# Optimization experiments

Measured on AMD Instinct MI355X. Metric: run time of the kernel, lower is better.

Reference implementation:

```python
import jax, jax.numpy as jnp
import numpy as np

BITS = 8

def _hilbert_distance(grid, bits=BITS):
    # Skilling's algorithm: 3D grid coords -> Hilbert curve distance. grid: [N,3] int64.
    X = grid.astype(np.int64).copy()
    n = X.shape[1]
    M = 1 << (bits - 1)
    Q = M
    while Q > 1:
        P = Q - 1
        for i in range(n):
            hi = (X[:, i] & Q) != 0
            X[:, 0] = np.where(hi, X[:, 0] ^ P, X[:, 0])
            t = np.where(hi, 0, (X[:, 0] ^ X[:, i]) & P)
            X[:, 0] ^= t
            X[:, i] ^= t
        Q >>= 1
    for i in range(1, n):
        X[:, i] ^= X[:, i - 1]
    t = np.zeros(X.shape[0], dtype=np.int64)
    Q = M
    while Q > 1:
        t = np.where((X[:, n - 1] & Q) != 0, t ^ (Q - 1), t)
        Q >>= 1
    X ^= t[:, None]
    h = np.zeros(X.shape[0], dtype=np.int64)
    for b in range(bits - 1, -1, -1):
        for i in range(n):
            h = (h << 1) | ((X[:, i] >> b) & 1)
    return h

def _orders(x_np, bits=BITS):
    B, N, _ = x_np.shape
    oh = np.zeros((B, N), dtype=np.int64)
    ot = np.zeros((B, N), dtype=np.int64)
    gmax = (1 << bits) - 1
    for b in range(B):
        pts = x_np[b]
        mins, maxs = pts.min(0), pts.max(0)
        span = np.maximum(maxs - mins, 1e-6)
        norm = (pts - mins) / span
        g = np.clip(norm * gmax, 0, gmax).astype(np.int64)
        oh[b] = np.argsort(_hilbert_distance(g, bits), kind='stable')
        gt = np.clip(norm[:, ::-1] * gmax, 0, gmax).astype(np.int64)
        ot[b] = np.argsort(_hilbert_distance(gt, bits), kind='stable')
    return oh, ot

def setup_inputs() -> dict:
    key = jax.random.key(0)
    ks = jax.random.split(key, 12)
    B, N, E = 4, 2048, 128
    NB, DS, DC, EXP, NC = 2, 16, 4, 2, 40
    DI = E * EXP
    DR = max(1, (E + 15) // 16)
    x = jax.random.normal(ks[0], (B, N, 3), jnp.float32)
    oh, ot = _orders(np.asarray(x))
    # dt_proj bias = softplus^-1(dt), dt ~ LogUniform(1e-3, 0.1)
    dt = jnp.exp(jax.random.uniform(ks[1], (NB, DI)) * (np.log(0.1) - np.log(0.001)) + np.log(0.001))
    dtproj_b = dt + jnp.log(-jnp.expm1(-dt))
    return dict(
        x=x,
        order_h=jnp.asarray(oh), order_t=jnp.asarray(ot),
        pe_w=jax.random.normal(ks[2], (E, 3)) * 0.3, pe_b=jnp.zeros((E,)),
        gamma=jnp.ones((2, E)), beta=jnp.zeros((2, E)),
        ln_g=jnp.ones((NB, E)), ln_b=jnp.zeros((NB, E)),
        inproj_w=jax.random.normal(ks[3], (NB, 2 * DI, E)) * (E ** -0.5),
        conv_w=jax.random.normal(ks[4], (NB, DI, DC)) * 0.3,
        conv_b=jnp.zeros((NB, DI)),
        xproj_w=jax.random.normal(ks[5], (NB, DR + 2 * DS, DI)) * (DI ** -0.5),
        dtproj_w=jax.random.normal(ks[6], (NB, DI, DR)) * (DR ** -0.5),
        dtproj_b=dtproj_b,
        A_log=jnp.tile(jnp.log(jnp.arange(1, DS + 1, dtype=jnp.float32))[None, None], (NB, DI, 1)),
        Dp=jnp.ones((NB, DI)),
        outproj_w=jax.random.normal(ks[7], (NB, E, DI)) * (DI ** -0.5),
        hn_g=jnp.ones((E,)), hn_b=jnp.zeros((E,)),
        fc_w=jax.random.normal(ks[8], (NC, E)) * (E ** -0.5),
        fc_b=jnp.zeros((NC,)),
    )

def _ln(x, g, b):
    m = jnp.mean(x, -1, keepdims=True)
    v = jnp.mean((x - m) ** 2, -1, keepdims=True)
    return (x - m) / jnp.sqrt(v + 1e-5) * g + b

def _block(h, g, bb, inw, cw, cb, xw, dtw, dtb, Alog, Dv, outw):
    B, L, E = h.shape
    DI, DC = cw.shape
    DR = dtw.shape[1]
    DS = Alog.shape[1]
    xn = _ln(h, g, bb)
    uz = xn @ inw.T                       # [B, L, 2*DI]
    u, z = uz[..., :DI], uz[..., DI:]
    # depthwise causal conv (kernel DC, left pad DC-1)
    up = jnp.pad(u, ((0, 0), (DC - 1, 0), (0, 0)))
    uc = cb + sum(up[:, k:k + L, :] * cw[:, k] for k in range(DC))
    uc = jax.nn.silu(uc)
    xdbl = uc @ xw.T                      # [B, L, DR+2*DS]
    dt = xdbl[..., :DR]
    Bv = xdbl[..., DR:DR + DS]
    Cv = xdbl[..., DR + DS:]
    delta = jax.nn.softplus(dt @ dtw.T + dtb)  # [B, L, DI]
    A = -jnp.exp(Alog)                    # [DI, DS]
    def step(hst, xs):
        d, ut, bt, ct = xs                # [B,DI],[B,DI],[B,DS],[B,DS]
        hst = jnp.exp(d[:, :, None] * A[None]) * hst + (d * ut)[:, :, None] * bt[:, None, :]
        y = jnp.einsum('bds,bs->bd', hst, ct) + Dv * ut
        return hst, y
    h0 = jnp.zeros((B, DI, DS), h.dtype)
    _, ys = jax.lax.scan(step, h0, (delta.transpose(1, 0, 2), uc.transpose(1, 0, 2),
                                    Bv.transpose(1, 0, 2), Cv.transpose(1, 0, 2)))
    y = ys.transpose(1, 0, 2) * jax.nn.silu(z)
    return h + y @ outw.T

def reference(x, order_h, order_t, pe_w, pe_b, gamma, beta, ln_g, ln_b,
              inproj_w, conv_w, conv_b, xproj_w, dtproj_w, dtproj_b,
              A_log, Dp, outproj_w, hn_g, hn_b, fc_w, fc_b):
    pts_h = jnp.take_along_axis(x, order_h[..., None], axis=1)
    pts_t = jnp.take_along_axis(x, order_t[..., None], axis=1)
    th = (pts_h @ pe_w.T + pe_b) * gamma[0] + beta[0]
    tt = (pts_t @ pe_w.T + pe_b) * gamma[1] + beta[1]
    h = jnp.concatenate([th, tt], axis=1)  # [B, 2N, E]
    for i in range(ln_g.shape[0]):
        h = _block(h, ln_g[i], ln_b[i], inproj_w[i], conv_w[i], conv_b[i], xproj_w[i],
                   dtproj_w[i], dtproj_b[i], A_log[i], Dp[i], outproj_w[i])
    h = _ln(h, hn_g, hn_b)
    return h.mean(axis=1) @ fc_w.T + fc_b
```

## Files before the change

kernel.cpp:

```cpp
#include <hip/hip_runtime.h>
#include <hip/hip_bf16.h>
#include <math.h>

#define BATCH 4
#define NPTS  2048
#define L     4096
#define E     128
#define DI    256
#define DS    16
#define DRR   8
#define DCV   4
#define NBLK  2
#define NC    40
#define XDW   40
#define ROWS  (BATCH*L)
#define CH    32
#define NCH   128

typedef unsigned short u16;
typedef short short8 __attribute__((ext_vector_type(8)));
typedef float f32x4v __attribute__((ext_vector_type(4)));

__device__ __forceinline__ u16 f2bf(float x) {
  unsigned u = __float_as_uint(x);
  u = u + 0x7FFFu + ((u >> 16) & 1u);
  return (u16)(u >> 16);
}
__device__ __forceinline__ float bf2f(u16 h) {
  return __uint_as_float(((unsigned)h) << 16);
}
__device__ __forceinline__ float softplusf(float x) {
  if (x > 20.f) return x;
  float t = __builtin_amdgcn_exp2f(x * 1.44269504f);
  return 0.69314718f * __builtin_amdgcn_logf(1.f + t);
}

__global__ void embed_ln_split(const float* __restrict__ x,
                               const int* __restrict__ oh, const int* __restrict__ ot,
                               const float* __restrict__ pe_w, const float* __restrict__ pe_b,
                               const float* __restrict__ gamma, const float* __restrict__ beta,
                               const float* __restrict__ g, const float* __restrict__ bb,
                               float* __restrict__ h, u16* __restrict__ dhi, u16* __restrict__ dlo) {
  int wave = threadIdx.x >> 6;
  int lane = threadIdx.x & 63;
  int row = blockIdx.x * 4 + wave;
  int n = row % L;
  int b = row / L;
  int gi = (n >= NPTS) ? 1 : 0;
  int nn = n - gi * NPTS;
  int src = gi ? ot[b * NPTS + nn] : oh[b * NPTS + nn];
  const float* xp = x + ((size_t)b * NPTS + src) * 3;
  float p0 = xp[0], p1 = xp[1], p2 = xp[2];
  int e0 = lane, e1 = lane + 64;
  float v0 = pe_b[e0] + p0 * pe_w[e0 * 3] + p1 * pe_w[e0 * 3 + 1] + p2 * pe_w[e0 * 3 + 2];
  float v1 = pe_b[e1] + p0 * pe_w[e1 * 3] + p1 * pe_w[e1 * 3 + 1] + p2 * pe_w[e1 * 3 + 2];
  v0 = v0 * gamma[gi * E + e0] + beta[gi * E + e0];
  v1 = v1 * gamma[gi * E + e1] + beta[gi * E + e1];
  size_t base = (size_t)row * E;
  h[base + e0] = v0;
  h[base + e1] = v1;
  float s1 = v0 + v1, s2 = v0 * v0 + v1 * v1;
  #pragma unroll
  for (int off = 32; off > 0; off >>= 1) {
    s1 += __shfl_xor(s1, off);
    s2 += __shfl_xor(s2, off);
  }
  float m = s1 * (1.0f / E);
  float var = s2 * (1.0f / E) - m * m;
  float inv = rsqrtf(var + 1e-5f);
  float o0 = (v0 - m) * inv * g[e0] + bb[e0];
  float o1 = (v1 - m) * inv * g[e1] + bb[e1];
  u16 h0 = f2bf(o0), h1 = f2bf(o1);
  dhi[base + e0] = h0; dhi[base + e1] = h1;
  dlo[base + e0] = f2bf(o0 - bf2f(h0));
  dlo[base + e1] = f2bf(o1 - bf2f(h1));
}

__global__ void split_all(const float* __restrict__ inproj, const float* __restrict__ outw,
                          const float* __restrict__ xw,
                          u16* __restrict__ wihi, u16* __restrict__ wilo,
                          u16* __restrict__ wohi, u16* __restrict__ wolo,
                          u16* __restrict__ wxhi, u16* __restrict__ wxlo) {
  const int n1 = NBLK * 2 * DI * E;
  const int n2 = NBLK * E * DI;
  const int n3 = NBLK * XDW * DI;
  int i = blockIdx.x * 256 + threadIdx.x;
  if (i < n1) {
    float v = inproj[i];
    u16 h = f2bf(v);
    wihi[i] = h; wilo[i] = f2bf(v - bf2f(h));
  } else if (i < n1 + n2) {
    int j = i - n1;
    float v = outw[j];
    u16 h = f2bf(v);
    wohi[j] = h; wolo[j] = f2bf(v - bf2f(h));
  } else if (i < n1 + n2 + n3) {
    int j = i - n1 - n2;
    float v = xw[j];
    u16 h = f2bf(v);
    wxhi[j] = h; wxlo[j] = f2bf(v - bf2f(h));
  }
}

template<int BN, int ACC>
__global__ __launch_bounds__(256)
void mfma_gemm_lds(const u16* __restrict__ Ahi, const u16* __restrict__ Alo,
                   const u16* __restrict__ Bhi, const u16* __restrict__ Blo,
                   float* __restrict__ C, int M, int N, int K, int ldc) {
  constexpr int BM = 128, BK = 64, PITCH = 72;
  constexpr int MSUB = (BN == 128) ? 4 : 2;
  constexpr int NSUB = 4;
  __shared__ u16 sA[2][BM][PITCH];
  __shared__ u16 sB[2][BN][PITCH];
  int tid = threadIdx.x;
  int wave = tid >> 6, lane = tid & 63, quad = lane >> 4, l16 = lane & 15;
  int rowBase = blockIdx.x * BM, colBase = blockIdx.y * BN;
  int wrow = (BN == 128) ? (wave >> 1) * 64 : wave * 32;
  int wcol = (BN == 128) ? (wave & 1) * 64 : 0;
  f32x4v acc[MSUB][NSUB] = {};
  for (int k0 = 0; k0 < K; k0 += BK) {
    #pragma unroll
    for (int hl = 0; hl < 2; hl++) {
      const u16* srcA = hl ? Alo : Ahi;
      #pragma unroll
      for (int c = 0; c < BM * 8 / 256; c++) {
        int ch = c * 256 + tid;
        int row = ch >> 3, kc = ch & 7;
        float4 v = *(const float4*)(srcA + (size_t)(rowBase + row) * K + k0 + kc * 8);
        *(float4*)&sA[hl][row][kc * 8] = v;
      }
      const u16* srcB = hl ? Blo : Bhi;
      #pragma unroll
      for (int c = 0; c < BN * 8 / 256; c++) {
        int ch = c * 256 + tid;
        int row = ch >> 3, kc = ch & 7;
        float4 v = *(const float4*)(srcB + (size_t)(colBase + row) * K + k0 + kc * 8);
        *(float4*)&sB[hl][row][kc * 8] = v;
      }
    }
    __syncthreads();
    short8 afh[MSUB][2], afl[MSUB][2];
    #pragma unroll
    for (int i = 0; i < MSUB; i++)
      #pragma unroll
      for (int kf = 0; kf < 2; kf++) {
        afh[i][kf] = *(const short8*)&sA[0][wrow + i * 16 + l16][kf * 32 + quad * 8];
        afl[i][kf] = *(const short8*)&sA[1][wrow + i * 16 + l16][kf * 32 + quad * 8];
      }
    #pragma unroll
    for (int j = 0; j < NSUB; j++)
      #pragma unroll
      for (int kf = 0; kf < 2; kf++) {
        short8 bh = *(const short8*)&sB[0][wcol + j * 16 + l16][kf * 32 + quad * 8];
        short8 bl = *(const short8*)&sB[1][wcol + j * 16 + l16][kf * 32 + quad * 8];
        #pragma unroll
        for (int i = 0; i < MSUB; i++) {
          acc[i][j] = __builtin_amdgcn_mfma_f32_16x16x32_bf16(afh[i][kf], bh, acc[i][j], 0, 0, 0);
          acc[i][j] = __builtin_amdgcn_mfma_f32_16x16x32_bf16(afh[i][kf], bl, acc[i][j], 0, 0, 0);
          acc[i][j] = __builtin_amdgcn_mfma_f32_16x16x32_bf16(afl[i][kf], bh, acc[i][j], 0, 0, 0);
        }
      }
    __syncthreads();
  }
  int orow0 = rowBase + wrow + quad * 4;
  #pragma unroll
  for (int i = 0; i < MSUB; i++) {
    #pragma unroll
    for (int j = 0; j < NSUB; j++) {
      int cc = colBase + wcol + j * 16 + l16;
      #pragma unroll
      for (int r = 0; r < 4; r++) {
        size_t idx = (size_t)(orow0 + i * 16 + r) * ldc + cc;
        if (ACC) C[idx] += acc[i][j][r];
        else     C[idx] = acc[i][j][r];
      }
    }
  }
}

__global__ __launch_bounds__(256)
void conv_xproj(const float* __restrict__ uz, const float* __restrict__ cw,
                const float* __restrict__ cb,
                const u16* __restrict__ xwhi, const u16* __restrict__ xwlo,
                float* __restrict__ xdbl) {
  constexpr int RB = 16, UPITCH = DI + 8;
  __shared__ u16 sUhi[RB][UPITCH];
  __shared__ u16 sUlo[RB][UPITCH];
  int d = threadIdx.x;
  int r0 = blockIdx.x * RB;
  int t0 = r0 % L;
  const size_t US = 2 * DI;
  float w0 = cw[d * DCV], w1 = cw[d * DCV + 1], w2 = cw[d * DCV + 2], w3 = cw[d * DCV + 3];
  float bias = cb[d];
  float uwin[RB + 3];
  #pragma unroll
  for (int j = 0; j < RB + 3; j++) {
    int t = t0 + j - 3;
    uwin[j] = (t >= 0) ? uz[(size_t)(r0 + j - 3) * US + d] : 0.f;
  }
  #pragma unroll
  for (int j = 0; j < RB; j++) {
    float a = bias + w0 * uwin[j] + w1 * uwin[j + 1] + w2 * uwin[j + 2] + w3 * uwin[j + 3];
    float v = a / (1.f + __expf(-a));
    u16 hh = f2bf(v);
    sUhi[j][d] = hh;
    sUlo[j][d] = f2bf(v - bf2f(hh));
  }
  __syncthreads();
  int wave = threadIdx.x >> 6, lane = threadIdx.x & 63;
  int quad = lane >> 4, l16 = lane & 15;
  if (wave < 3) {
    int col = wave * 16 + l16;
    int colc = (col < XDW) ? col : 0;
    const u16* bhp = xwhi + (size_t)colc * DI;
    const u16* blp = xwlo + (size_t)colc * DI;
    f32x4v acc = {};
    #pragma unroll
    for (int ks = 0; ks < DI / 32; ks++) {
      short8 ah = *(const short8*)&sUhi[l16][ks * 32 + quad * 8];
      short8 al = *(const short8*)&sUlo[l16][ks * 32 + quad * 8];
      short8 bh = *(const short8*)(bhp + ks * 32 + quad * 8);
      short8 bl = *(const short8*)(blp + ks * 32 + quad * 8);
      acc = __builtin_amdgcn_mfma_f32_16x16x32_bf16(ah, bh, acc, 0, 0, 0);
      acc = __builtin_amdgcn_mfma_f32_16x16x32_bf16(ah, bl, acc, 0, 0, 0);
      acc = __builtin_amdgcn_mfma_f32_16x16x32_bf16(al, bh, acc, 0, 0, 0);
      acc = __builtin_amdgcn_mfma_f32_16x16x32_bf16(al, bl, acc, 0, 0, 0);
    }
    if (col < XDW) {
      #pragma unroll
      for (int r = 0; r < 4; r++)
        xdbl[(size_t)(r0 + quad * 4 + r) * XDW + col] = acc[r];
    }
  }
}

__global__ __launch_bounds__(256, 4)
void scan_passA(const float* __restrict__ uz, const float* __restrict__ xdbl,
                const float* __restrict__ dtw, const float* __restrict__ dtb,
                const float* __restrict__ A_log,
                const float* __restrict__ cw, const float* __restrict__ cb,
                float* __restrict__ hloc, float* __restrict__ sumd) {
  int b = blockIdx.x / NCH, c = blockIdx.x % NCH;
  int d = threadIdx.x;
  __shared__ float Bsh[CH][DS];
  __shared__ float Dsh[CH][DRR];
  for (int i = threadIdx.x; i < CH * DS; i += 256) {
    int tt = i >> 4, s = i & 15;
    Bsh[tt][s] = xdbl[((size_t)b * L + c * CH + tt) * XDW + DRR + s];
  }
  {
    int i = threadIdx.x;
    int td = i >> 3, q = i & 7;
    Dsh[td][q] = xdbl[((size_t)b * L + c * CH + td) * XDW + q];
  }
  const size_t US = 2 * DI;
  const float* up = uz + ((size_t)b * L + c * CH) * US + d;
  float cw0 = cw[d * DCV], cw1 = cw[d * DCV + 1], cw2 = cw[d * DCV + 2], cw3 = cw[d * DCV + 3];
  float cbias = cb[d];
  float um0, um1, um2;
  if (c == 0) { um0 = um1 = um2 = 0.f; }
  else {
    um0 = up[-3 * (ptrdiff_t)US];
    um1 = up[-2 * (ptrdiff_t)US];
    um2 = up[-1 * (ptrdiff_t)US];
  }
  float ucur = up[0];
  float Av[DS];
  #pragma unroll
  for (int s = 0; s < DS; s++) Av[s] = -__expf(A_log[d * DS + s]);
  float4 wd0 = *(const float4*)(dtw + d * DRR);
  float4 wd1 = *(const float4*)(dtw + d * DRR + 4);
  float dbias = dtb[d];
  __syncthreads();
  float st[DS] = {};
  float sd = 0.f;
  #pragma unroll
  for (int t0 = 0; t0 < CH; t0++) {
    float unext = (t0 + 1 < CH) ? up[(size_t)(t0 + 1) * US] : 0.f;
    float a = cbias + cw0 * um0 + cw1 * um1 + cw2 * um2 + cw3 * ucur;
    float utv = a / (1.f + __expf(-a));
    um0 = um1; um1 = um2; um2 = ucur; ucur = unext;
    float4 D0 = *(const float4*)&Dsh[t0][0];
    float4 D1 = *(const float4*)&Dsh[t0][4];
    float v = dbias + D0.x * wd0.x + D0.y * wd0.y + D0.z * wd0.z + D0.w * wd0.w
                    + D1.x * wd1.x + D1.y * wd1.y + D1.z * wd1.z + D1.w * wd1.w;
    float dl = softplusf(v);
    sd += dl;
    float du = dl * utv;
    float4 B0 = *(const float4*)&Bsh[t0][0];
    float4 B1 = *(const float4*)&Bsh[t0][4];
    float4 B2 = *(const float4*)&Bsh[t0][8];
    float4 B3 = *(const float4*)&Bsh[t0][12];
    float Bv[DS] = {B0.x, B0.y, B0.z, B0.w, B1.x, B1.y, B1.z, B1.w,
                    B2.x, B2.y, B2.z, B2.w, B3.x, B3.y, B3.z, B3.w};
    #pragma unroll
    for (int s = 0; s < DS; s++) {
      float aa = __expf(dl * Av[s]);
      st[s] = aa * st[s] + du * Bv[s];
    }
  }
  size_t base = (((size_t)b * NCH + c) * DI + d) * DS;
  *(float4*)&hloc[base + 0]  = float4{st[0], st[1], st[2], st[3]};
  *(float4*)&hloc[base + 4]  = float4{st[4], st[5], st[6], st[7]};
  *(float4*)&hloc[base + 8]  = float4{st[8], st[9], st[10], st[11]};
  *(float4*)&hloc[base + 12] = float4{st[12], st[13], st[14], st[15]};
  sumd[((size_t)b * NCH + c) * DI + d] = sd;
}

#define PB_G 16
__global__ __launch_bounds__(64)
void scan_passB(const float* __restrict__ A_log, const float* __restrict__ hloc,
                const float* __restrict__ sumd, float* __restrict__ hinit) {
  int tid = threadIdx.x;
  int dgroup = blockIdx.x % (DI / 4);
  int b = blockIdx.x / (DI / 4);
  int d = dgroup * 4 + (tid >> 4);
  int s = tid & 15;
  float Av = -__expf(A_log[d * DS + s]);
  size_t off = (size_t)b * NCH * DI * DS + dgroup * 64 + tid;
  size_t soff = (size_t)b * NCH * DI + d;
  const size_t HST = (size_t)DI * DS;
  float bv[PB_G], sd[PB_G], bvn[PB_G], sdn[PB_G];
  #pragma unroll
  for (int j = 0; j < PB_G; j++) {
    bv[j] = hloc[off + j * HST];
    sd[j] = sumd[soff + j * DI];
  }
  float X = 0.f;
  for (int g = 0; g < NCH / PB_G; g++) {
    if (g + 1 < NCH / PB_G) {
      #pragma unroll
      for (int j = 0; j < PB_G; j++) {
        bvn[j] = hloc[off + (j + PB_G) * HST];
        sdn[j] = sumd[soff + (j + PB_G) * DI];
      }
    }
    #pragma unroll
    for (int j = 0; j < PB_G; j++) {
      float a = __expf(Av * sd[j]);
      hinit[off + j * HST] = X;
      X = a * X + bv[j];
    }
    #pragma unroll
    for (int j = 0; j < PB_G; j++) { bv[j] = bvn[j]; sd[j] = sdn[j]; }
    off += PB_G * HST;
    soff += PB_G * DI;
  }
}

template<int VARIANT>
__global__ __launch_bounds__(256, 2)
void scan_passC_out(const float* __restrict__ uz, const float* __restrict__ xdbl,
                    const float* __restrict__ dtw, const float* __restrict__ dtb,
                    const float* __restrict__ A_log, const float* __restrict__ Dp,
                    const float* __restrict__ cw, const float* __restrict__ cb,
                    const float* __restrict__ hinit,
                    const u16* __restrict__ wohi, const u16* __restrict__ wolo,
                    float* __restrict__ h, const float* __restrict__ g,
                    const float* __restrict__ bb, u16* __restrict__ dhi,
                    u16* __restrict__ dlo, float* __restrict__ partial) {
  constexpr int YP = DI + 8;
  constexpr int HP = E + 4;
  int b = blockIdx.x / NCH, c = blockIdx.x % NCH;
  int d = threadIdx.x;
  __shared__ float Bsh[CH][DS];
  __shared__ float Csh[CH][DS];
  __shared__ float Dsh[CH][DRR];
  __shared__ u16 sYhi[CH][YP];
  __shared__ u16 sYlo[CH][YP];
  __shared__ float hsm[CH][HP];
  __shared__ float red[4][E];
  for (int i = threadIdx.x; i < CH * DS; i += 256) {
    int tt = i >> 4, s = i & 15;
    size_t rb = ((size_t)b * L + c * CH + tt) * XDW;
    Bsh[tt][s] = xdbl[rb + DRR + s];
    Csh[tt][s] = xdbl[rb + DRR + DS + s];
  }
  {
    int i = threadIdx.x;
    int td = i >> 3, q = i & 7;
    Dsh[td][q] = xdbl[((size_t)b * L + c * CH + td) * XDW + q];
  }
  const size_t US = 2 * DI;
  const float* up = uz + ((size_t)b * L + c * CH) * US + d;
  const float* zp = up + DI;
  float cw0 = cw[d * DCV], cw1 = cw[d * DCV + 1], cw2 = cw[d * DCV + 2], cw3 = cw[d * DCV + 3];
  float cbias = cb[d];
  float um0, um1, um2;
  if (c == 0) { um0 = um1 = um2 = 0.f; }
  else {
    um0 = up[-3 * (ptrdiff_t)US];
    um1 = up[-2 * (ptrdiff_t)US];
    um2 = up[-1 * (ptrdiff_t)US];
  }
  float ucur = up[0];
  float zcur = zp[0];
  float st[DS];
  size_t hbase = (((size_t)b * NCH + c) * DI + d) * DS;
  {
    float4 h0 = *(const float4*)&hinit[hbase + 0];
    float4 h1 = *(const float4*)&hinit[hbase + 4];
    float4 h2 = *(const float4*)&hinit[hbase + 8];
    float4 h3 = *(const float4*)&hinit[hbase + 12];
    st[0]=h0.x; st[1]=h0.y; st[2]=h0.z; st[3]=h0.w;
    st[4]=h1.x; st[5]=h1.y; st[6]=h1.z; st[7]=h1.w;
    st[8]=h2.x; st[9]=h2.y; st[10]=h2.z; st[11]=h2.w;
    st[12]=h3.x; st[13]=h3.y; st[14]=h3.z; st[15]=h3.w;
  }
  float Av[DS];
  #pragma unroll
  for (int s = 0; s < DS; s++) Av[s] = -__expf(A_log[d * DS + s]);
  float4 wd0 = *(const float4*)(dtw + d * DRR);
  float4 wd1 = *(const float4*)(dtw + d * DRR + 4);
  float dbias = dtb[d];
  float Dv = Dp[d];
  __syncthreads();
  #pragma unroll 8
  for (int t0 = 0; t0 < CH; t0++) {
    float unext = (t0 + 1 < CH) ? up[(size_t)(t0 + 1) * US] : 0.f;
    float znext = (t0 + 1 < CH) ? zp[(size_t)(t0 + 1) * US] : 0.f;
    float a = cbias + cw0 * um0 + cw1 * um1 + cw2 * um2 + cw3 * ucur;
    float utv = a / (1.f + __expf(-a));
    um0 = um1; um1 = um2; um2 = ucur; ucur = unext;
    float4 D0 = *(const float4*)&Dsh[t0][0];
    float4 D1 = *(const float4*)&Dsh[t0][4];
    float v = dbias + D0.x * wd0.x + D0.y * wd0.y + D0.z * wd0.z + D0.w * wd0.w
                    + D1.x * wd1.x + D1.y * wd1.y + D1.z * wd1.z + D1.w * wd1.w;
    float dl = softplusf(v);
    float du = dl * utv;
    float acc = Dv * utv;
    float4 B0 = *(const float4*)&Bsh[t0][0];
    float4 B1 = *(const float4*)&Bsh[t0][4];
    float4 B2 = *(const float4*)&Bsh[t0][8];
    float4 B3 = *(const float4*)&Bsh[t0][12];
    float4 C0 = *(const float4*)&Csh[t0][0];
    float4 C1 = *(const float4*)&Csh[t0][4];
    float4 C2 = *(const float4*)&Csh[t0][8];
    float4 C3 = *(const float4*)&Csh[t0][12];
    float Bv[DS] = {B0.x, B0.y, B0.z, B0.w, B1.x, B1.y, B1.z, B1.w,
                    B2.x, B2.y, B2.z, B2.w, B3.x, B3.y, B3.z, B3.w};
    float Cv[DS] = {C0.x, C0.y, C0.z, C0.w, C1.x, C1.y, C1.z, C1.w,
                    C2.x, C2.y, C2.z, C2.w, C3.x, C3.y, C3.z, C3.w};
    #pragma unroll
    for (int s = 0; s < DS; s++) {
      float aa = __expf(dl * Av[s]);
      st[s] = aa * st[s] + du * Bv[s];
      acc += st[s] * Cv[s];
    }
    float zz = zcur; zcur = znext;
    float yv = acc * (zz / (1.f + __expf(-zz)));
    u16 hh = f2bf(yv);
    sYhi[t0][d] = hh;
    sYlo[t0][d] = f2bf(yv - bf2f(hh));
  }
  __syncthreads();
  int wave = d >> 6, lane = d & 63, quad = lane >> 4, l16 = lane & 15;
  f32x4v oacc[2][2] = {};
  #pragma unroll
  for (int ks = 0; ks < DI / 32; ks++) {
    short8 a0h = *(const short8*)&sYhi[l16][ks * 32 + quad * 8];
    short8 a0l = *(const short8*)&sYlo[l16][ks * 32 + quad * 8];
    short8 a1h = *(const short8*)&sYhi[16 + l16][ks * 32 + quad * 8];
    short8 a1l = *(const short8*)&sYlo[16 + l16][ks * 32 + quad * 8];
    #pragma unroll
    for (int j = 0; j < 2; j++) {
      int col = wave * 32 + j * 16 + l16;
      short8 bh = *(const short8*)(wohi + (size_t)col * DI + ks * 32 + quad * 8);
      short8 bl = *(const short8*)(wolo + (size_t)col * DI + ks * 32 + quad * 8);
      oacc[0][j] = __builtin_amdgcn_mfma_f32_16x16x32_bf16(a0h, bh, oacc[0][j], 0, 0, 0);
      oacc[0][j] = __builtin_amdgcn_mfma_f32_16x16x32_bf16(a0h, bl, oacc[0][j], 0, 0, 0);
      oacc[0][j] = __builtin_amdgcn_mfma_f32_16x16x32_bf16(a0l, bh, oacc[0][j], 0, 0, 0);
      oacc[1][j] = __builtin_amdgcn_mfma_f32_16x16x32_bf16(a1h, bh, oacc[1][j], 0, 0, 0);
      oacc[1][j] = __builtin_amdgcn_mfma_f32_16x16x32_bf16(a1h, bl, oacc[1][j], 0, 0, 0);
      oacc[1][j] = __builtin_amdgcn_mfma_f32_16x16x32_bf16(a1l, bh, oacc[1][j], 0, 0, 0);
    }
  }
  size_t rr0 = (size_t)b * L + c * CH;
  #pragma unroll
  for (int i = 0; i < 2; i++) {
    #pragma unroll
    for (int j = 0; j < 2; j++) {
      int col = wave * 32 + j * 16 + l16;
      #pragma unroll
      for (int r = 0; r < 4; r++) {
        int row = i * 16 + quad * 4 + r;
        float v = h[(rr0 + row) * E + col] + oacc[i][j][r];
        hsm[row][col] = v;
        if (VARIANT == 0) h[(rr0 + row) * E + col] = v;
      }
    }
  }
  __syncthreads();
  float g0 = g[lane], g1 = g[lane + 64], b0 = bb[lane], b1 = bb[lane + 64];
  float pa0 = 0.f, pa1 = 0.f;
  for (int jj = 0; jj < 8; jj++) {
    int row = wave * 8 + jj;
    float x0 = hsm[row][lane], x1 = hsm[row][lane + 64];
    float s1 = x0 + x1, s2 = x0 * x0 + x1 * x1;
    #pragma unroll
    for (int off = 32; off > 0; off >>= 1) {
      s1 += __shfl_xor(s1, off);
      s2 += __shfl_xor(s2, off);
    }
    float m = s1 * (1.0f / E);
    float var = s2 * (1.0f / E) - m * m;
    float inv = rsqrtf(var + 1e-5f);
    float o0 = (x0 - m) * inv * g0 + b0;
    float o1 = (x1 - m) * inv * g1 + b1;
    if (VARIANT == 0) {
      size_t base = (rr0 + row) * E;
      u16 h0 = f2bf(o0), h1 = f2bf(o1);
      dhi[base + lane]      = h0;
      dhi[base + lane + 64] = h1;
      dlo[base + lane]      = f2bf(o0 - bf2f(h0));
      dlo[base + lane + 64] = f2bf(o1 - bf2f(h1));
    } else {
      pa0 += o0; pa1 += o1;
    }
  }
  if (VARIANT == 1) {
    red[wave][lane]      = pa0;
    red[wave][lane + 64] = pa1;
    __syncthreads();
    if (wave == 0) {
      #pragma unroll
      for (int half = 0; half < 2; half++) {
        int e = lane + half * 64;
        partial[(size_t)blockIdx.x * E + e] =
            red[0][e] + red[1][e] + red[2][e] + red[3][e];
      }
    }
  }
}

__global__ __launch_bounds__(256)
void fc_reduce(const float* __restrict__ partial, float* __restrict__ hmean) {
  int w = blockIdx.x * 4 + (threadIdx.x >> 6);
  int lane = threadIdx.x & 63;
  int b = w >> 7, e = w & 127;
  float s = partial[((size_t)b * NCH + lane) * E + e]
          + partial[((size_t)b * NCH + 64 + lane) * E + e];
  #pragma unroll
  for (int off = 32; off > 0; off >>= 1) s += __shfl_xor(s, off);
  if (lane == 0) hmean[w] = s;
}

__global__ __launch_bounds__(256)
void fc_final(const float* __restrict__ hmean, const float* __restrict__ fcw,
              const float* __restrict__ fcb, float* __restrict__ out) {
  constexpr int WP = E + 4;
  __shared__ float hm[BATCH * E];
  __shared__ float wsm[NC * WP];
  for (int i = threadIdx.x; i < BATCH * E; i += 256) hm[i] = hmean[i];
  for (int i = threadIdx.x; i < NC * E; i += 256) {
    int o = i >> 7, e = i & 127;
    wsm[o * WP + e] = fcw[i];
  }
  __syncthreads();
  int i = threadIdx.x;
  if (i < BATCH * NC) {
    int b = i / NC, o = i % NC;
    float acc = 0.f;
    #pragma unroll 8
    for (int e = 0; e < E; e++) acc += hm[b * E + e] * wsm[o * WP + e];
    out[i] = acc * (1.f / L) + fcb[o];
  }
}

extern "C" void kernel_launch(void* const* d_in, const int* in_sizes, int n_in,
                              void* d_out, int out_size, void* d_ws, size_t ws_size,
                              hipStream_t stream) {
  const float* x      = (const float*)d_in[0];
  const int*   oh     = (const int*)d_in[1];
  const int*   ot     = (const int*)d_in[2];
  const float* pe_w   = (const float*)d_in[3];
  const float* pe_b   = (const float*)d_in[4];
  const float* gamma  = (const float*)d_in[5];
  const float* beta   = (const float*)d_in[6];
  const float* ln_g   = (const float*)d_in[7];
  const float* ln_b   = (const float*)d_in[8];
  const float* inproj = (const float*)d_in[9];
  const float* conv_w = (const float*)d_in[10];
  const float* conv_b = (const float*)d_in[11];
  const float* xproj  = (const float*)d_in[12];
  const float* dtw    = (const float*)d_in[13];
  const float* dtb    = (const float*)d_in[14];
  const float* A_log  = (const float*)d_in[15];
  const float* Dp     = (const float*)d_in[16];
  const float* outw   = (const float*)d_in[17];
  const float* hn_g   = (const float*)d_in[18];
  const float* hn_b   = (const float*)d_in[19];
  const float* fc_w   = (const float*)d_in[20];
  const float* fc_b   = (const float*)d_in[21];
  float* out = (float*)d_out;

  char* ws = (char*)d_ws;
  size_t off = 0;
  auto alloc = [&](size_t bytes) { size_t o = off; off += (bytes + 255) & ~(size_t)255; return o; };
  float* h     = (float*)(ws + alloc((size_t)ROWS * E * 4));
  u16*   xnhi  = (u16*)  (ws + alloc((size_t)ROWS * E * 2));
  u16*   xnlo  = (u16*)  (ws + alloc((size_t)ROWS * E * 2));
  float* uz    = (float*)(ws + alloc((size_t)ROWS * 2 * DI * 4));
  float* xdbl  = (float*)(ws + alloc((size_t)ROWS * XDW * 4));
  float* hloc  = (float*)(ws + alloc((size_t)BATCH * NCH * DI * DS * 4));
  float* sumd  = (float*)(ws + alloc((size_t)BATCH * NCH * DI * 4));
  u16*   wihi  = (u16*)  (ws + alloc((size_t)NBLK * 2 * DI * E * 2));
  u16*   wilo  = (u16*)  (ws + alloc((size_t)NBLK * 2 * DI * E * 2));
  u16*   wohi  = (u16*)  (ws + alloc((size_t)NBLK * E * DI * 2));
  u16*   wolo  = (u16*)  (ws + alloc((size_t)NBLK * E * DI * 2));
  u16*   wxhi  = (u16*)  (ws + alloc((size_t)NBLK * XDW * DI * 2));
  u16*   wxlo  = (u16*)  (ws + alloc((size_t)NBLK * XDW * DI * 2));
  float* partial = (float*)(ws + alloc((size_t)BATCH * NCH * E * 4));
  float* hmean = (float*)(ws + alloc((size_t)BATCH * E * 4));
  float* hinit = hloc;

  embed_ln_split<<<ROWS / 4, 256, 0, stream>>>(x, oh, ot, pe_w, pe_b, gamma, beta,
                                               ln_g, ln_b, h, xnhi, xnlo);
  const int nsplit = NBLK * 2 * DI * E + NBLK * E * DI + NBLK * XDW * DI;
  split_all<<<(nsplit + 255) / 256, 256, 0, stream>>>(inproj, outw, xproj,
                                                      wihi, wilo, wohi, wolo, wxhi, wxlo);

  for (int i = 0; i < NBLK; i++) {
    dim3 g1(ROWS / 128, (2 * DI) / 128);
    mfma_gemm_lds<128, 0><<<g1, 256, 0, stream>>>(xnhi, xnlo,
                                                  wihi + (size_t)i * 2 * DI * E, wilo + (size_t)i * 2 * DI * E,
                                                  uz, ROWS, 2 * DI, E, 2 * DI);

    conv_xproj<<<ROWS / 16, 256, 0, stream>>>(uz, conv_w + (size_t)i * DI * DCV, conv_b + i * DI,
                                              wxhi + (size_t)i * XDW * DI, wxlo + (size_t)i * XDW * DI,
                                              xdbl);

    scan_passA<<<BATCH * NCH, 256, 0, stream>>>(uz, xdbl, dtw + (size_t)i * DI * DRR, dtb + i * DI,
                                                A_log + (size_t)i * DI * DS,
                                                conv_w + (size_t)i * DI * DCV, conv_b + i * DI,
                                                hloc, sumd);
    scan_passB<<<BATCH * (DI / 4), 64, 0, stream>>>(A_log + (size_t)i * DI * DS, hloc, sumd, hinit);

    if (i == 0) {
      scan_passC_out<0><<<BATCH * NCH, 256, 0, stream>>>(uz, xdbl, dtw + (size_t)i * DI * DRR, dtb + i * DI,
                                                         A_log + (size_t)i * DI * DS, Dp + i * DI,
                                                         conv_w + (size_t)i * DI * DCV, conv_b + i * DI,
                                                         hinit,
                                                         wohi + (size_t)i * E * DI, wolo + (size_t)i * E * DI,
                                                         h, ln_g + (i + 1) * E, ln_b + (i + 1) * E,
                                                         xnhi, xnlo, partial);
    } else {
      scan_passC_out<1><<<BATCH * NCH, 256, 0, stream>>>(uz, xdbl, dtw + (size_t)i * DI * DRR, dtb + i * DI,
                                                         A_log + (size_t)i * DI * DS, Dp + i * DI,
                                                         conv_w + (size_t)i * DI * DCV, conv_b + i * DI,
                                                         hinit,
                                                         wohi + (size_t)i * E * DI, wolo + (size_t)i * E * DI,
                                                         h, hn_g, hn_b,
                                                         xnhi, xnlo, partial);
    }
  }

  fc_reduce<<<128, 256, 0, stream>>>(partial, hmean);
  fc_final<<<1, 256, 0, stream>>>(hmean, fc_w, fc_b, out);
}
```

Before: 293.9 us.

## Fuse conv+xproj into scan pass A and use exp power ladder for A

Merges the conv_xproj kernel into the first scan pass, so each chunk block computes the conv+SiLU activations, runs the x_proj MFMA in shared memory and feeds delta/B straight into the local scan. This drops one launch and the xdbl round trip for pass A, while still writing xdbl for pass C. Both scan passes also gain a runtime check for whether A equals -(s+1), the standard S4D-real init. When it does, the 16 exponentials per step are replaced by one exp plus repeated multiplies. The fast path depends on the weights matching that init, and the fused kernel has more registers and LDS with fewer blocks per CU.

```diff
diff --git a/kernel.cpp b/kernel.cpp
--- a/kernel.cpp
+++ b/kernel.cpp
@@ -33,6 +33,22 @@
   if (x > 20.f) return x;
   float t = __builtin_amdgcn_exp2f(x * 1.44269504f);
   return 0.69314718f * __builtin_amdgcn_logf(1.f + t);
+}
+
+__device__ __forceinline__ void exp_ladder(bool fastE, float dl,
+                                           const float* __restrict__ Av,
+                                           float* __restrict__ aa) {
+  if (fastE) {
+    float e1 = __expf(-dl);
+    float e2 = e1 * e1, e4 = e2 * e2, e8 = e4 * e4;
+    aa[0] = e1;        aa[1] = e2;        aa[2] = e2 * e1;   aa[3] = e4;
+    aa[4] = e4 * e1;   aa[5] = e4 * e2;   aa[6] = aa[5] * e1; aa[7] = e8;
+    aa[8] = e8 * e1;   aa[9] = e8 * e2;   aa[10] = aa[9] * e1; aa[11] = e8 * e4;
+    aa[12] = aa[11] * e1; aa[13] = aa[11] * e2; aa[14] = aa[13] * e1; aa[15] = e8 * e8;
+  } else {
+    #pragma unroll
+    for (int s = 0; s < DS; s++) aa[s] = __expf(dl * Av[s]);
+  }
 }
 
 __global__ void embed_ln_split(const float* __restrict__ x,
@@ -178,81 +194,21 @@
   }
 }
 
-__global__ __launch_bounds__(256)
-void conv_xproj(const float* __restrict__ uz, const float* __restrict__ cw,
-                const float* __restrict__ cb,
-                const u16* __restrict__ xwhi, const u16* __restrict__ xwlo,
-                float* __restrict__ xdbl) {
-  constexpr int RB = 16, UPITCH = DI + 8;
-  __shared__ u16 sUhi[RB][UPITCH];
-  __shared__ u16 sUlo[RB][UPITCH];
-  int d = threadIdx.x;
-  int r0 = blockIdx.x * RB;
-  int t0 = r0 % L;
-  const size_t US = 2 * DI;
-  float w0 = cw[d * DCV], w1 = cw[d * DCV + 1], w2 = cw[d * DCV + 2], w3 = cw[d * DCV + 3];
-  float bias = cb[d];
-  float uwin[RB + 3];
-  #pragma unroll
-  for (int j = 0; j < RB + 3; j++) {
-    int t = t0 + j - 3;
-    uwin[j] = (t >= 0) ? uz[(size_t)(r0 + j - 3) * US + d] : 0.f;
-  }
-  #pragma unroll
-  for (int j = 0; j < RB; j++) {
-    float a = bias + w0 * uwin[j] + w1 * uwin[j + 1] + w2 * uwin[j + 2] + w3 * uwin[j + 3];
-    float v = a / (1.f + __expf(-a));
-    u16 hh = f2bf(v);
-    sUhi[j][d] = hh;
-    sUlo[j][d] = f2bf(v - bf2f(hh));
-  }
-  __syncthreads();
-  int wave = threadIdx.x >> 6, lane = threadIdx.x & 63;
-  int quad = lane >> 4, l16 = lane & 15;
-  if (wave < 3) {
-    int col = wave * 16 + l16;
-    int colc = (col < XDW) ? col : 0;
-    const u16* bhp = xwhi + (size_t)colc * DI;
-    const u16* blp = xwlo + (size_t)colc * DI;
-    f32x4v acc = {};
-    #pragma unroll
-    for (int ks = 0; ks < DI / 32; ks++) {
-      short8 ah = *(const short8*)&sUhi[l16][ks * 32 + quad * 8];
-      short8 al = *(const short8*)&sUlo[l16][ks * 32 + quad * 8];
-      short8 bh = *(const short8*)(bhp + ks * 32 + quad * 8);
-      short8 bl = *(const short8*)(blp + ks * 32 + quad * 8);
-      acc = __builtin_amdgcn_mfma_f32_16x16x32_bf16(ah, bh, acc, 0, 0, 0);
-      acc = __builtin_amdgcn_mfma_f32_16x16x32_bf16(ah, bl, acc, 0, 0, 0);
-      acc = __builtin_amdgcn_mfma_f32_16x16x32_bf16(al, bh, acc, 0, 0, 0);
-      acc = __builtin_amdgcn_mfma_f32_16x16x32_bf16(al, bl, acc, 0, 0, 0);
-    }
-    if (col < XDW) {
-      #pragma unroll
-      for (int r = 0; r < 4; r++)
-        xdbl[(size_t)(r0 + quad * 4 + r) * XDW + col] = acc[r];
-    }
-  }
-}
-
-__global__ __launch_bounds__(256, 4)
-void scan_passA(const float* __restrict__ uz, const float* __restrict__ xdbl,
-                const float* __restrict__ dtw, const float* __restrict__ dtb,
-                const float* __restrict__ A_log,
-                const float* __restrict__ cw, const float* __restrict__ cb,
-                float* __restrict__ hloc, float* __restrict__ sumd) {
+__global__ __launch_bounds__(256, 2)
+void scan_passA_cx(const float* __restrict__ uz,
+                   const float* __restrict__ cw, const float* __restrict__ cb,
+                   const u16* __restrict__ xwhi, const u16* __restrict__ xwlo,
+                   const float* __restrict__ dtw, const float* __restrict__ dtb,
+                   const float* __restrict__ A_log,
+                   float* __restrict__ xdbl,
+                   float* __restrict__ hloc, float* __restrict__ sumd) {
+  constexpr int UPITCH = DI + 8;
+  constexpr int XP = 48;
+  __shared__ u16 sUhi[CH][UPITCH];
+  __shared__ u16 sUlo[CH][UPITCH];
+  __shared__ float xsm[CH][XP];
   int b = blockIdx.x / NCH, c = blockIdx.x % NCH;
   int d = threadIdx.x;
-  __shared__ float Bsh[CH][DS];
-  __shared__ float Dsh[CH][DRR];
-  for (int i = threadIdx.x; i < CH * DS; i += 256) {
-    int tt = i >> 4, s = i & 15;
-    Bsh[tt][s] = xdbl[((size_t)b * L + c * CH + tt) * XDW + DRR + s];
-  }
-  {
-    int i = threadIdx.x;
-    int td = i >> 3, q = i & 7;
-    Dsh[td][q] = xdbl[((size_t)b * L + c * CH + td) * XDW + q];
-  }
   const size_t US = 2 * DI;
   const float* up = uz + ((size_t)b * L + c * CH) * US + d;
   float cw0 = cw[d * DCV], cw1 = cw[d * DCV + 1], cw2 = cw[d * DCV + 2], cw3 = cw[d * DCV + 3];
@@ -265,39 +221,83 @@
     um2 = up[-1 * (ptrdiff_t)US];
   }
   float ucur = up[0];
+  float utv[CH];
+  #pragma unroll
+  for (int j = 0; j < CH; j++) {
+    float unext = (j + 1 < CH) ? up[(size_t)(j + 1) * US] : 0.f;
+    float a = cbias + cw0 * um0 + cw1 * um1 + cw2 * um2 + cw3 * ucur;
+    float v = a / (1.f + __expf(-a));
+    um0 = um1; um1 = um2; um2 = ucur; ucur = unext;
+    utv[j] = v;
+    u16 hh = f2bf(v);
+    sUhi[j][d] = hh;
+    sUlo[j][d] = f2bf(v - bf2f(hh));
+  }
+  __syncthreads();
+  int wave = d >> 6, lane = d & 63, quad = lane >> 4, l16 = lane & 15;
+  if (wave < 3) {
+    int col = wave * 16 + l16;
+    int colc = (col < XDW) ? col : 0;
+    const u16* bhp = xwhi + (size_t)colc * DI;
+    const u16* blp = xwlo + (size_t)colc * DI;
+    f32x4v acc[2] = {};
+    #pragma unroll
+    for (int ks = 0; ks < DI / 32; ks++) {
+      short8 bh = *(const short8*)(bhp + ks * 32 + quad * 8);
+      short8 bl = *(const short8*)(blp + ks * 32 + quad * 8);
+      #pragma unroll
+      for (int i = 0; i < 2; i++) {
+        short8 ah = *(const short8*)&sUhi[i * 16 + l16][ks * 32 + quad * 8];
+        short8 al = *(const short8*)&sUlo[i * 16 + l16][ks * 32 + quad * 8];
+        acc[i] = __builtin_amdgcn_mfma_f32_16x16x32_bf16(ah, bh, acc[i], 0, 0, 0);
+        acc[i] = __builtin_amdgcn_mfma_f32_16x16x32_bf16(ah, bl, acc[i], 0, 0, 0);
+        acc[i] = __builtin_amdgcn_mfma_f32_16x16x32_bf16(al, bh, acc[i], 0, 0, 0);
+        acc[i] = __builtin_amdgcn_mfma_f32_16x16x32_bf16(al, bl, acc[i], 0, 0, 0);
+      }
+    }
+    size_t rbase = (size_t)b * L + c * CH;
+    #pragma unroll
+    for (int i = 0; i < 2; i++) {
+      #pragma unroll
+      for (int r = 0; r < 4; r++) {
+        int row = i * 16 + quad * 4 + r;
+        xsm[row][col] = acc[i][r];
+        if (col < XDW) xdbl[(rbase + row) * XDW + col] = acc[i][r];
+      }
+    }
+  }
+  __syncthreads();
   float Av[DS];
   #pragma unroll
   for (int s = 0; s < DS; s++) Av[s] = -__expf(A_log[d * DS + s]);
+  bool fastE = true;
+  #pragma unroll
+  for (int s = 0; s < DS; s++)
+    fastE = fastE && (fabsf(Av[s] + (float)(s + 1)) <= 1e-3f * (s + 1));
   float4 wd0 = *(const float4*)(dtw + d * DRR);
   float4 wd1 = *(const float4*)(dtw + d * DRR + 4);
   float dbias = dtb[d];
-  __syncthreads();
   float st[DS] = {};
   float sd = 0.f;
   #pragma unroll
   for (int t0 = 0; t0 < CH; t0++) {
-    float unext = (t0 + 1 < CH) ? up[(size_t)(t0 + 1) * US] : 0.f;
-    float a = cbias + cw0 * um0 + cw1 * um1 + cw2 * um2 + cw3 * ucur;
-    float utv = a / (1.f + __expf(-a));
-    um0 = um1; um1 = um2; um2 = ucur; ucur = unext;
-    float4 D0 = *(const float4*)&Dsh[t0][0];
-    float4 D1 = *(const float4*)&Dsh[t0][4];
+    float4 D0 = *(const float4*)&xsm[t0][0];
+    float4 D1 = *(const float4*)&xsm[t0][4];
     float v = dbias + D0.x * wd0.x + D0.y * wd0.y + D0.z * wd0.z + D0.w * wd0.w
                     + D1.x * wd1.x + D1.y * wd1.y + D1.z * wd1.z + D1.w * wd1.w;
     float dl = softplusf(v);
     sd += dl;
-    float du = dl * utv;
-    float4 B0 = *(const float4*)&Bsh[t0][0];
-    float4 B1 = *(const float4*)&Bsh[t0][4];
-    float4 B2 = *(const float4*)&Bsh[t0][8];
-    float4 B3 = *(const float4*)&Bsh[t0][12];
+    float du = dl * utv[t0];
+    float aa[DS];
+    exp_ladder(fastE, dl, Av, aa);
+    float4 B0 = *(const float4*)&xsm[t0][DRR + 0];
+    float4 B1 = *(const float4*)&xsm[t0][DRR + 4];
+    float4 B2 = *(const float4*)&xsm[t0][DRR + 8];
+    float4 B3 = *(const float4*)&xsm[t0][DRR + 12];
     float Bv[DS] = {B0.x, B0.y, B0.z, B0.w, B1.x, B1.y, B1.z, B1.w,
                     B2.x, B2.y, B2.z, B2.w, B3.x, B3.y, B3.z, B3.w};
     #pragma unroll
-    for (int s = 0; s < DS; s++) {
-      float aa = __expf(dl * Av[s]);
-      st[s] = aa * st[s] + du * Bv[s];
-    }
+    for (int s = 0; s < DS; s++) st[s] = aa[s] * st[s] + du * Bv[s];
   }
   size_t base = (((size_t)b * NCH + c) * DI + d) * DS;
   *(float4*)&hloc[base + 0]  = float4{st[0], st[1], st[2], st[3]};
@@ -410,6 +410,10 @@
   float Av[DS];
   #pragma unroll
   for (int s = 0; s < DS; s++) Av[s] = -__expf(A_log[d * DS + s]);
+  bool fastE = true;
+  #pragma unroll
+  for (int s = 0; s < DS; s++)
+    fastE = fastE && (fabsf(Av[s] + (float)(s + 1)) <= 1e-3f * (s + 1));
   float4 wd0 = *(const float4*)(dtw + d * DRR);
   float4 wd1 = *(const float4*)(dtw + d * DRR + 4);
   float dbias = dtb[d];
@@ -429,6 +433,8 @@
     float dl = softplusf(v);
     float du = dl * utv;
     float acc = Dv * utv;
+    float aa[DS];
+    exp_ladder(fastE, dl, Av, aa);
     float4 B0 = *(const float4*)&Bsh[t0][0];
     float4 B1 = *(const float4*)&Bsh[t0][4];
     float4 B2 = *(const float4*)&Bsh[t0][8];
@@ -443,8 +449,7 @@
                     C2.x, C2.y, C2.z, C2.w, C3.x, C3.y, C3.z, C3.w};
     #pragma unroll
     for (int s = 0; s < DS; s++) {
-      float aa = __expf(dl * Av[s]);
-      st[s] = aa * st[s] + du * Bv[s];
+      st[s] = aa[s] * st[s] + du * Bv[s];
       acc += st[s] * Cv[s];
     }
     float zz = zcur; zcur = znext;
@@ -626,14 +631,12 @@
                                                   wihi + (size_t)i * 2 * DI * E, wilo + (size_t)i * 2 * DI * E,
                                                   uz, ROWS, 2 * DI, E, 2 * DI);
 
-    conv_xproj<<<ROWS / 16, 256, 0, stream>>>(uz, conv_w + (size_t)i * DI * DCV, conv_b + i * DI,
-                                              wxhi + (size_t)i * XDW * DI, wxlo + (size_t)i * XDW * DI,
-                                              xdbl);
-
-    scan_passA<<<BATCH * NCH, 256, 0, stream>>>(uz, xdbl, dtw + (size_t)i * DI * DRR, dtb + i * DI,
-                                                A_log + (size_t)i * DI * DS,
-                                                conv_w + (size_t)i * DI * DCV, conv_b + i * DI,
-                                                hloc, sumd);
+    scan_passA_cx<<<BATCH * NCH, 256, 0, stream>>>(uz,
+                                                   conv_w + (size_t)i * DI * DCV, conv_b + i * DI,
+                                                   wxhi + (size_t)i * XDW * DI, wxlo + (size_t)i * XDW * DI,
+                                                   dtw + (size_t)i * DI * DRR, dtb + i * DI,
+                                                   A_log + (size_t)i * DI * DS,
+                                                   xdbl, hloc, sumd);
     scan_passB<<<BATCH * (DI / 4), 64, 0, stream>>>(A_log + (size_t)i * DI * DS, hloc, sumd, hinit);
 
     if (i == 0) {
```

Result: slower. 730.3 us (+148.5%).
